# Optimization experiments

Hardware: AMD Instinct MI355X
Metric: run time of the kernel (lower is better)

Reference implementation:

```python
import jax, jax.numpy as jnp
import numpy as np

B, S, H, NH = 4, 2048, 256, 8
EPS = 1e-5


def setup_inputs() -> dict:
    key = jax.random.key(0)
    ks = jax.random.split(key, 12)
    p = lambda k, shape: (jax.random.normal(k, shape, jnp.float32) * 0.02)
    return {
        "x": jax.random.normal(ks[0], (B, S, H), jnp.float32),
        "lengths": jax.random.randint(ks[1], (B,), 0, S).astype(jnp.int32),
        "atten_in": jnp.zeros((1,), jnp.float32),
        "Wq": p(ks[2], (H, H)), "bq": jnp.zeros((H,), jnp.float32),
        "Wk": p(ks[3], (H, H)), "bk": jnp.zeros((H,), jnp.float32),
        "Wv": p(ks[4], (H, H)), "bv": jnp.zeros((H,), jnp.float32),
        "W1": p(ks[5], (H, H)), "b1": jnp.zeros((H,), jnp.float32),
        "W2": p(ks[6], (H, H)), "b2": jnp.zeros((H,), jnp.float32),
        "g1": jnp.ones((H,), jnp.float32), "beta1": jnp.zeros((H,), jnp.float32),
        "g2": jnp.ones((H,), jnp.float32), "beta2": jnp.zeros((H,), jnp.float32),
    }


def _layer_norm(x, g, b):
    mu = x.mean(-1, keepdims=True)
    var = ((x - mu) ** 2).mean(-1, keepdims=True)
    return (x - mu) / jnp.sqrt(var + EPS) * g + b


def reference(x, lengths, atten_in, Wq, bq, Wk, bk, Wv, bv, W1, b1, W2, b2, g1, beta1, g2, beta2):
    Bx, Sx, Hx = x.shape
    hd = Hx // NH
    # QKV projections, split heads -> [B, NH, S, hd]
    q = (x @ Wq + bq).reshape(Bx, Sx, NH, hd).transpose(0, 2, 1, 3)
    k = (x @ Wk + bk).reshape(Bx, Sx, NH, hd).transpose(0, 2, 1, 3)
    v = (x @ Wv + bv).reshape(Bx, Sx, NH, hd).transpose(0, 2, 1, 3)
    # NOTE: original scales by sqrt(hidden_size), not sqrt(head_dim)
    scores = jnp.einsum('bhqd,bhkd->bhqk', q, k) / np.sqrt(Hx).astype(np.float32)
    pos = jnp.arange(Sx)
    causal = pos[:, None] >= pos[None, :]                     # [S, S]
    row_ok = pos[None, :] < lengths[:, None]                  # [B, S]: mask query rows >= length
    head_ok = jnp.arange(NH)[None, :] < lengths[:, None]      # [B, NH]: original loop masks heads >= length
    mask = causal[None, None] & row_ok[:, None, :, None] & head_ok[:, :, None, None]
    neg = jnp.finfo(scores.dtype).min
    logits = jnp.where(mask, scores, neg)
    atten = jax.nn.softmax(logits, axis=-1)
    # original: masked_fill((atten > 0) == False, 0) -> fully masked rows (NaN in torch) become 0
    atten = jnp.where(mask, atten, 0.0)
    row_valid = mask.any(-1, keepdims=True)
    atten = jnp.where(row_valid, atten, 0.0)
    out = jnp.einsum('bhqk,bhkd->bhqd', atten, v).transpose(0, 2, 1, 3).reshape(Bx, Sx, Hx)
    atten_mean = atten.mean(axis=1)  # [B, S, S], detached in original
    out_1 = x + out  # dropout p=0 / eval mode -> identity
    out_1_norm = _layer_norm(out_1, g1, beta1)
    ff = jax.nn.gelu(out_1_norm @ W1 + b1, approximate=False) @ W2 + b2
    y_prim = _layer_norm(out_1_norm + ff, g2, beta2)
    return (y_prim, lengths, atten_mean)
```

## Files before the change

### kernel.cpp

```cpp
#include <hip/hip_runtime.h>
#include <math.h>

#define BB 4
#define SS 2048
#define HH 256
#define NHH 8
#define EPSV 1e-5f
#define NC 8
#define CHW (SS/NC)
#define NCO 4
#define QPRE 0.09016844005556021f

#if __has_builtin(__builtin_amdgcn_exp2f)
#define EXP2F(x) __builtin_amdgcn_exp2f(x)
#else
#define EXP2F(x) __expf((x) * 0.6931471805599453f)
#endif

typedef unsigned short ushortT;
typedef __attribute__((ext_vector_type(8))) short bf16x8;
typedef __attribute__((ext_vector_type(4))) float f32x4;

__device__ inline ushortT f2bf(float f) {
    union { float f; unsigned int u; } x; x.f = f;
    unsigned int r = x.u + 0x7FFFu + ((x.u >> 16) & 1u);
    return (ushortT)(r >> 16);
}
__device__ inline ushortT f2bf_rz(float f) {
    union { float f; unsigned int u; } x; x.f = f;
    return (ushortT)(x.u >> 16);
}
__device__ inline float bf2f(ushortT u) {
    union { unsigned int i; float f; } x; x.i = ((unsigned int)u) << 16;
    return x.f;
}

__global__ __launch_bounds__(256) void prep(const float* __restrict__ x,
        ushortT* __restrict__ xb, const int* __restrict__ L,
        float* __restrict__ out_len,
        const float* __restrict__ Wa, const float* __restrict__ Wb,
        const float* __restrict__ Wc, const float* __restrict__ Wd,
        const float* __restrict__ We, ushortT* __restrict__ Wtb) {
    const int bid = blockIdx.x;
    if (bid < 1024) {
        const int i = (bid * 256 + threadIdx.x) << 3;
        float4 v0 = *(const float4*)(x + i);
        float4 v1 = *(const float4*)(x + i + 4);
        bf16x8 o;
        o[0] = (short)f2bf(v0.x); o[1] = (short)f2bf(v0.y);
        o[2] = (short)f2bf(v0.z); o[3] = (short)f2bf(v0.w);
        o[4] = (short)f2bf(v1.x); o[5] = (short)f2bf(v1.y);
        o[6] = (short)f2bf(v1.z); o[7] = (short)f2bf(v1.w);
        *(bf16x8*)(xb + i) = o;
        if (bid == 0 && threadIdx.x < BB) out_len[threadIdx.x] = (float)L[threadIdx.x];
        return;
    }
    const int wb = bid - 1024;
    const int z = wb >> 6;
    const int rem = wb & 63;
    const int k0 = (rem >> 3) << 5, n0 = (rem & 7) << 5;
    const float* W = (z == 0) ? Wa : (z == 1) ? Wb : (z == 2) ? Wc : (z == 3) ? Wd : We;
    __shared__ float tile[32][33];
    const int t = threadIdx.x;
    const int r = t >> 3, c4 = (t & 7) << 2;
    float4 v = *(const float4*)(W + (size_t)(k0 + r) * HH + n0 + c4);
    tile[r][c4+0] = v.x; tile[r][c4+1] = v.y; tile[r][c4+2] = v.z; tile[r][c4+3] = v.w;
    __syncthreads();
    ushort4 o;
    o.x = f2bf(tile[c4+0][r]); o.y = f2bf(tile[c4+1][r]);
    o.z = f2bf(tile[c4+2][r]); o.w = f2bf(tile[c4+3][r]);
    *(ushort4*)(Wtb + (size_t)z * 65536 + (size_t)(n0 + r) * HH + k0 + c4) = o;
}

__global__ __launch_bounds__(256) void gemm_qkv(const ushortT* __restrict__ A,
        const ushortT* __restrict__ Wtb,
        const float* __restrict__ bq, const float* __restrict__ bk,
        const float* __restrict__ bv,
        ushortT* __restrict__ Qb, ushortT* __restrict__ Kb,
        ushortT* __restrict__ Vt) {
    __shared__ ushortT As[64][264];
    __shared__ ushortT Ws[64][264];
    const int wsel = blockIdx.y >> 2;
    const int n0 = (blockIdx.y & 3) << 6;
    const ushortT* Wt = Wtb + (size_t)wsel * 65536;
    const float* bias = (wsel == 0) ? bq : (wsel == 1) ? bk : bv;
    const int tid = threadIdx.x;
    const int m0 = blockIdx.x << 6;
    #pragma unroll
    for (int t = 0; t < 8; ++t) {
        const int f = t * 256 + tid;
        const int r = f >> 5;
        const int cc = (f & 31) << 3;
        *(bf16x8*)&As[r][cc] = *(const bf16x8*)(A + (size_t)(m0 + r) * HH + cc);
        *(bf16x8*)&Ws[r][cc] = *(const bf16x8*)(Wt + (size_t)(n0 + r) * HH + cc);
    }
    __syncthreads();
    const int w = tid >> 6, lane = tid & 63;
    const int lg = lane >> 4, lc = lane & 15;
    const int wr = (w & 1) << 5, wc = (w >> 1) << 5;
    f32x4 acc[2][2];
    const f32x4 z4 = {0.f, 0.f, 0.f, 0.f};
    acc[0][0] = z4; acc[0][1] = z4; acc[1][0] = z4; acc[1][1] = z4;
    #pragma unroll
    for (int k0 = 0; k0 < 256; k0 += 32) {
        bf16x8 a0 = *(const bf16x8*)&As[wr + lc][k0 + lg*8];
        bf16x8 a1 = *(const bf16x8*)&As[wr + 16 + lc][k0 + lg*8];
        bf16x8 b0 = *(const bf16x8*)&Ws[wc + lc][k0 + lg*8];
        bf16x8 b1 = *(const bf16x8*)&Ws[wc + 16 + lc][k0 + lg*8];
        acc[0][0] = __builtin_amdgcn_mfma_f32_16x16x32_bf16(a0, b0, acc[0][0], 0, 0, 0);
        acc[0][1] = __builtin_amdgcn_mfma_f32_16x16x32_bf16(a0, b1, acc[0][1], 0, 0, 0);
        acc[1][0] = __builtin_amdgcn_mfma_f32_16x16x32_bf16(a1, b0, acc[1][0], 0, 0, 0);
        acc[1][1] = __builtin_amdgcn_mfma_f32_16x16x32_bf16(a1, b1, acc[1][1], 0, 0, 0);
    }
    ushortT* Out = (wsel == 0) ? Qb : Kb;
    #pragma unroll
    for (int RH = 0; RH < 2; ++RH)
        #pragma unroll
        for (int CH = 0; CH < 2; ++CH) {
            const int col = n0 + wc + CH*16 + lc;
            const float bvv = bias[col];
            float v[4];
            #pragma unroll
            for (int r = 0; r < 4; ++r) {
                v[r] = acc[RH][CH][r] + bvv;
                if (wsel == 0) v[r] *= QPRE;
            }
            if (wsel < 2) {
                #pragma unroll
                for (int r = 0; r < 4; ++r) {
                    const int row = m0 + wr + RH*16 + lg*4 + r;
                    Out[(size_t)row * HH + col] = f2bf(v[r]);
                }
            } else {
                const int row0 = m0 + wr + RH*16 + lg*4;
                const int bidx = row0 >> 11, s0 = row0 & (SS - 1);
                ushort4 o;
                o.x = f2bf(v[0]); o.y = f2bf(v[1]); o.z = f2bf(v[2]); o.w = f2bf(v[3]);
                *(ushort4*)(Vt + ((size_t)(bidx * HH + col)) * SS + s0) = o;
            }
        }
}

template<int MODE>
__global__ __launch_bounds__(256) void gemm_mfma(const ushortT* __restrict__ A,
        const ushortT* __restrict__ Wt, const float* __restrict__ bias,
        void* __restrict__ Cv) {
    __shared__ ushortT As[64][264];
    __shared__ ushortT Ws[64][264];
    const int tid = threadIdx.x;
    const int m0 = blockIdx.x << 6;
    const int n0 = blockIdx.y << 6;
    #pragma unroll
    for (int t = 0; t < 8; ++t) {
        const int f = t * 256 + tid;
        const int r = f >> 5;
        const int cc = (f & 31) << 3;
        *(bf16x8*)&As[r][cc] = *(const bf16x8*)(A + (size_t)(m0 + r) * HH + cc);
        *(bf16x8*)&Ws[r][cc] = *(const bf16x8*)(Wt + (size_t)(n0 + r) * HH + cc);
    }
    __syncthreads();
    const int w = tid >> 6, lane = tid & 63;
    const int lg = lane >> 4, lc = lane & 15;
    const int wr = (w & 1) << 5, wc = (w >> 1) << 5;
    f32x4 acc[2][2];
    const f32x4 z4 = {0.f, 0.f, 0.f, 0.f};
    acc[0][0] = z4; acc[0][1] = z4; acc[1][0] = z4; acc[1][1] = z4;
    #pragma unroll
    for (int k0 = 0; k0 < 256; k0 += 32) {
        bf16x8 a0 = *(const bf16x8*)&As[wr + lc][k0 + lg*8];
        bf16x8 a1 = *(const bf16x8*)&As[wr + 16 + lc][k0 + lg*8];
        bf16x8 b0 = *(const bf16x8*)&Ws[wc + lc][k0 + lg*8];
        bf16x8 b1 = *(const bf16x8*)&Ws[wc + 16 + lc][k0 + lg*8];
        acc[0][0] = __builtin_amdgcn_mfma_f32_16x16x32_bf16(a0, b0, acc[0][0], 0, 0, 0);
        acc[0][1] = __builtin_amdgcn_mfma_f32_16x16x32_bf16(a0, b1, acc[0][1], 0, 0, 0);
        acc[1][0] = __builtin_amdgcn_mfma_f32_16x16x32_bf16(a1, b0, acc[1][0], 0, 0, 0);
        acc[1][1] = __builtin_amdgcn_mfma_f32_16x16x32_bf16(a1, b1, acc[1][1], 0, 0, 0);
    }
    #pragma unroll
    for (int RH = 0; RH < 2; ++RH)
        #pragma unroll
        for (int CH = 0; CH < 2; ++CH) {
            const int col = n0 + wc + CH*16 + lc;
            const float bv = bias[col];
            #pragma unroll
            for (int r = 0; r < 4; ++r) {
                const int row = m0 + wr + RH*16 + lg*4 + r;
                float v = acc[RH][CH][r] + bv;
                if (MODE == 2) v = 0.5f * v * (1.0f + erff(v * 0.70710678118f));
                if (MODE == 0) ((float*)Cv)[(size_t)row * HH + col] = v;
                else           ((ushortT*)Cv)[(size_t)row * HH + col] = f2bf(v);
            }
        }
}

__global__ __launch_bounds__(512) void attn_sums(const ushortT* __restrict__ Qb,
        const ushortT* __restrict__ Kb, const int* __restrict__ lengths,
        float* __restrict__ Psum) {
    const int b = blockIdx.z, c = blockIdx.y;
    const int i0 = (63 - blockIdx.x) << 5;
    const int len = lengths[b];
    const int jmax = min(i0 + 31, len - 1);
    const int jstart = c * CHW;
    if (i0 >= len || jstart > jmax) return;
    const int tid = threadIdx.x;
    const int w = tid >> 6, lane = tid & 63;
    const int lg = lane >> 4, lc = lane & 15;
    bf16x8 qf[2];
    #pragma unroll
    for (int RH = 0; RH < 2; ++RH)
        qf[RH] = *(const bf16x8*)(Qb + ((size_t)(b * SS + i0 + RH*16 + lc)) * HH + w*32 + lg*8);
    const f32x4 z4 = {0.f, 0.f, 0.f, 0.f};
    float lsum[2][4] = {};
    const int jend = min(jstart + CHW - 32, (jmax >> 5) << 5);
    bf16x8 kf0 = *(const bf16x8*)(Kb + ((size_t)(b * SS + jstart + lc)) * HH + w*32 + lg*8);
    bf16x8 kf1 = *(const bf16x8*)(Kb + ((size_t)(b * SS + jstart + 16 + lc)) * HH + w*32 + lg*8);
    for (int j0 = jstart; j0 <= jend; j0 += 32) {
        bf16x8 ck0 = kf0, ck1 = kf1;
        if (j0 + 32 <= jend) {
            kf0 = *(const bf16x8*)(Kb + ((size_t)(b * SS + j0 + 32 + lc)) * HH + w*32 + lg*8);
            kf1 = *(const bf16x8*)(Kb + ((size_t)(b * SS + j0 + 48 + lc)) * HH + w*32 + lg*8);
        }
        f32x4 s[2][2];
        #pragma unroll
        for (int RH = 0; RH < 2; ++RH) {
            s[RH][0] = __builtin_amdgcn_mfma_f32_16x16x32_bf16(qf[RH], ck0, z4, 0, 0, 0);
            s[RH][1] = __builtin_amdgcn_mfma_f32_16x16x32_bf16(qf[RH], ck1, z4, 0, 0, 0);
        }
        if (j0 < i0) {
            #pragma unroll
            for (int RH = 0; RH < 2; ++RH)
                #pragma unroll
                for (int r = 0; r < 4; ++r)
                    #pragma unroll
                    for (int CH = 0; CH < 2; ++CH)
                        lsum[RH][r] += EXP2F(s[RH][CH][r]);
        } else {
            #pragma unroll
            for (int RH = 0; RH < 2; ++RH)
                #pragma unroll
                for (int r = 0; r < 4; ++r) {
                    const int row = i0 + RH*16 + lg*4 + r;
                    #pragma unroll
                    for (int CH = 0; CH < 2; ++CH) {
                        const int j = j0 + CH*16 + lc;
                        lsum[RH][r] += (j <= row) ? EXP2F(s[RH][CH][r]) : 0.f;
                    }
                }
        }
    }
    #pragma unroll
    for (int RH = 0; RH < 2; ++RH)
        #pragma unroll
        for (int r = 0; r < 4; ++r) {
            float v = lsum[RH][r];
            v += __shfl_xor(v, 1); v += __shfl_xor(v, 2);
            v += __shfl_xor(v, 4); v += __shfl_xor(v, 8);
            if (lc == 0)
                Psum[((size_t)(c * BB + b) * NHH + w) * SS + i0 + RH*16 + lg*4 + r] = v;
        }
}

__global__ __launch_bounds__(512) void attn_pv(const ushortT* __restrict__ Qb,
        const ushortT* __restrict__ Kb, const ushortT* __restrict__ Vt,
        const int* __restrict__ lengths, const float* __restrict__ Psum,
        ushortT* __restrict__ OPart, float* __restrict__ out_mean) {
    __shared__ __align__(16) ushortT Pb[2][NHH][32][40];
    __shared__ float invS[NHH][32];
    const int b = blockIdx.z, cg = blockIdx.y;
    const int i0 = (63 - blockIdx.x) << 5;
    const int len = lengths[b];
    const int tid = threadIdx.x;
    const int mr = tid >> 4, mc = (tid & 15) << 1;
    float* meanrow = out_mean + ((size_t)(b * SS + i0 + mr)) * SS + mc;
    const int T = (i0 < len) ? ((min(i0 + 31, len - 1) >> 5) + 1) : 0;
    for (int t = T + ((cg - T) & (NCO - 1)); t < 64; t += NCO)
        *(float2*)(meanrow + (t << 5)) = make_float2(0.f, 0.f);
    const int q = T >> 2, r = T & (NCO - 1);
    const int t0 = cg * q + min(cg, r);
    const int t1 = t0 + q + (cg < r ? 1 : 0);
    if (t0 >= t1) return;
    if (tid < NHH * 32) {
        const int hh = tid >> 5, row = i0 + (tid & 31);
        float rv = 0.f;
        if (row < len && hh < len) {
            float s = 0.f;
            const int ncv = (row >> 8) + 1;
            for (int c2 = 0; c2 < ncv; ++c2)
                s += Psum[((size_t)(c2 * BB + b) * NHH + hh) * SS + row];
            rv = (s > 0.f) ? 1.0f / s : 0.f;
        }
        invS[hh][tid & 31] = rv;
    }
    __syncthreads();
    const int w = tid >> 6, lane = tid & 63;
    const int lg = lane >> 4, lc = lane & 15;
    bf16x8 qf[2];
    #pragma unroll
    for (int RH = 0; RH < 2; ++RH)
        qf[RH] = *(const bf16x8*)(Qb + ((size_t)(b * SS + i0 + RH*16 + lc)) * HH + w*32 + lg*8);
    float invv[2][4];
    #pragma unroll
    for (int RH = 0; RH < 2; ++RH)
        #pragma unroll
        for (int r2 = 0; r2 < 4; ++r2)
            invv[RH][r2] = invS[w][RH*16 + lg*4 + r2];
    float invh8[NHH];
    #pragma unroll
    for (int hh = 0; hh < NHH; ++hh)
        invh8[hh] = invS[hh][mr] * 0.125f;
    const f32x4 z4 = {0.f, 0.f, 0.f, 0.f};
    f32x4 O[2][2];
    O[0][0] = z4; O[0][1] = z4; O[1][0] = z4; O[1][1] = z4;
    const int jstart = t0 << 5;
    bf16x8 kf0 = *(const bf16x8*)(Kb + ((size_t)(b * SS + jstart + lc)) * HH + w*32 + lg*8);
    bf16x8 kf1 = *(const bf16x8*)(Kb + ((size_t)(b * SS + jstart + 16 + lc)) * HH + w*32 + lg*8);
    bf16x8 vf0 = *(const bf16x8*)(Vt + ((size_t)(b * HH + w*32 + lc)) * SS + jstart + lg*8);
    bf16x8 vf1 = *(const bf16x8*)(Vt + ((size_t)(b * HH + w*32 + 16 + lc)) * SS + jstart + lg*8);
    int par = 0;
    for (int t = t0; t < t1; ++t) {
        const int j0 = t << 5;
        bf16x8 ck0 = kf0, ck1 = kf1, cv0 = vf0, cv1 = vf1;
        if (t + 1 < t1) {
            kf0 = *(const bf16x8*)(Kb + ((size_t)(b * SS + j0 + 32 + lc)) * HH + w*32 + lg*8);
            kf1 = *(const bf16x8*)(Kb + ((size_t)(b * SS + j0 + 48 + lc)) * HH + w*32 + lg*8);
            vf0 = *(const bf16x8*)(Vt + ((size_t)(b * HH + w*32 + lc)) * SS + j0 + 32 + lg*8);
            vf1 = *(const bf16x8*)(Vt + ((size_t)(b * HH + w*32 + 16 + lc)) * SS + j0 + 32 + lg*8);
        }
        f32x4 s[2][2];
        #pragma unroll
        for (int RH = 0; RH < 2; ++RH) {
            s[RH][0] = __builtin_amdgcn_mfma_f32_16x16x32_bf16(qf[RH], ck0, z4, 0, 0, 0);
            s[RH][1] = __builtin_amdgcn_mfma_f32_16x16x32_bf16(qf[RH], ck1, z4, 0, 0, 0);
        }
        if (j0 < i0) {
            #pragma unroll
            for (int RH = 0; RH < 2; ++RH)
                #pragma unroll
                for (int CH = 0; CH < 2; ++CH)
                    #pragma unroll
                    for (int r2 = 0; r2 < 4; ++r2)
                        Pb[par][w][RH*16 + lg*4 + r2][CH*16 + lc] =
                            f2bf_rz(EXP2F(s[RH][CH][r2]));
        } else {
            #pragma unroll
            for (int RH = 0; RH < 2; ++RH)
                #pragma unroll
                for (int CH = 0; CH < 2; ++CH)
                    #pragma unroll
                    for (int r2 = 0; r2 < 4; ++r2) {
                        const int row = i0 + RH*16 + lg*4 + r2;
                        const int j = j0 + CH*16 + lc;
                        Pb[par][w][RH*16 + lg*4 + r2][CH*16 + lc] =
                            (j <= row) ? f2bf_rz(EXP2F(s[RH][CH][r2])) : (ushortT)0;
                    }
        }
        __syncthreads();
        #pragma unroll
        for (int RH = 0; RH < 2; ++RH) {
            bf16x8 pa = *(const bf16x8*)&Pb[par][w][RH*16 + lc][lg*8];
            O[RH][0] = __builtin_amdgcn_mfma_f32_16x16x32_bf16(pa, cv0, O[RH][0], 0, 0, 0);
            O[RH][1] = __builtin_amdgcn_mfma_f32_16x16x32_bf16(pa, cv1, O[RH][1], 0, 0, 0);
        }
        float m0 = 0.f, m1 = 0.f;
        #pragma unroll
        for (int ww = 0; ww < NHH; ++ww) {
            ushort2 t2 = *(const ushort2*)&Pb[par][ww][mr][mc];
            m0 += bf2f(t2.x) * invh8[ww]; m1 += bf2f(t2.y) * invh8[ww];
        }
        *(float2*)(meanrow + (j0)) = make_float2(m0, m1);
        par ^= 1;
    }
    ushortT* op = OPart + (size_t)cg * ((size_t)BB * SS * HH);
    #pragma unroll
    for (int RH = 0; RH < 2; ++RH)
        #pragma unroll
        for (int DH = 0; DH < 2; ++DH)
            #pragma unroll
            for (int r2 = 0; r2 < 4; ++r2)
                op[((size_t)(b * SS + i0 + RH*16 + lg*4 + r2)) * HH + w*32 + DH*16 + lc] =
                    f2bf(O[RH][DH][r2] * invv[RH][r2]);
}

__global__ __launch_bounds__(256) void add_ln_attn(const float* __restrict__ x,
        const ushortT* __restrict__ OPart, const int* __restrict__ lengths,
        const float* __restrict__ g, const float* __restrict__ beta,
        float* __restrict__ out, ushortT* __restrict__ outb) {
    const int row = blockIdx.x;
    const int c = threadIdx.x;
    const int i = row & (SS - 1);
    const int len = lengths[row >> 11];
    const size_t base = (size_t)row * 256;
    float v = x[base + c];
    if (i < len) {
        const int ncv = min(NCO, (i >> 5) + 1);
        for (int cc = 0; cc < ncv; ++cc)
            v += bf2f(OPart[(size_t)cc * ((size_t)BB * SS * HH) + base + c]);
    }
    __shared__ float red[8];
    float s = v;
    #pragma unroll
    for (int o = 32; o; o >>= 1) s += __shfl_down(s, o, 64);
    const int wid = c >> 6, lane = c & 63;
    if (lane == 0) red[wid] = s;
    __syncthreads();
    float mu = (red[0] + red[1] + red[2] + red[3]) * 0.00390625f;
    float d = v - mu;
    float q = d * d;
    #pragma unroll
    for (int o = 32; o; o >>= 1) q += __shfl_down(q, o, 64);
    if (lane == 0) red[4 + wid] = q;
    __syncthreads();
    float var = (red[4] + red[5] + red[6] + red[7]) * 0.00390625f;
    float res = d * rsqrtf(var + EPSV) * g[c] + beta[c];
    out[base + c] = res;
    outb[base + c] = f2bf(res);
}

__global__ __launch_bounds__(256) void add_ln(const float* __restrict__ A,
        const float* __restrict__ Bv, const float* __restrict__ g,
        const float* __restrict__ beta, float* __restrict__ out) {
    const int row = blockIdx.x;
    const int c = threadIdx.x;
    const size_t base = (size_t)row * 256;
    float v = A[base + c] + Bv[base + c];
    __shared__ float red[8];
    float s = v;
    #pragma unroll
    for (int o = 32; o; o >>= 1) s += __shfl_down(s, o, 64);
    const int wid = c >> 6, lane = c & 63;
    if (lane == 0) red[wid] = s;
    __syncthreads();
    float mu = (red[0] + red[1] + red[2] + red[3]) * 0.00390625f;
    float d = v - mu;
    float q = d * d;
    #pragma unroll
    for (int o = 32; o; o >>= 1) q += __shfl_down(q, o, 64);
    if (lane == 0) red[4 + wid] = q;
    __syncthreads();
    float var = (red[4] + red[5] + red[6] + red[7]) * 0.00390625f;
    out[base + c] = d * rsqrtf(var + EPSV) * g[c] + beta[c];
}

extern "C" void kernel_launch(void* const* d_in, const int* in_sizes, int n_in,
                              void* d_out, int out_size, void* d_ws, size_t ws_size,
                              hipStream_t stream) {
    const float* x   = (const float*)d_in[0];
    const int* lengths = (const int*)d_in[1];
    const float* Wq  = (const float*)d_in[3];
    const float* bq  = (const float*)d_in[4];
    const float* Wk  = (const float*)d_in[5];
    const float* bk  = (const float*)d_in[6];
    const float* Wv  = (const float*)d_in[7];
    const float* bv  = (const float*)d_in[8];
    const float* W1  = (const float*)d_in[9];
    const float* b1  = (const float*)d_in[10];
    const float* W2  = (const float*)d_in[11];
    const float* b2  = (const float*)d_in[12];
    const float* g1  = (const float*)d_in[13];
    const float* be1 = (const float*)d_in[14];
    const float* g2  = (const float*)d_in[15];
    const float* be2 = (const float*)d_in[16];
    float* out = (float*)d_out;
    float* ws  = (float*)d_ws;

    const size_t NELT = (size_t)BB * SS * HH;
    const size_t M1 = 1024 * 1024;

    ushortT* xb  = (ushortT*)ws;
    float*   Psum = ws;
    ushortT* Qbf = (ushortT*)(ws + M1);
    ushortT* Kbf = (ushortT*)(ws + 2 * M1);
    ushortT* Vtb = (ushortT*)(ws + 3 * M1);
    float*   X1N  = ws + 4 * M1;
    ushortT* Wtb = (ushortT*)(ws + 6 * M1);
    ushortT* OPart = (ushortT*)(ws + 7 * M1);
    ushortT* X1Nb = (ushortT*)ws;
    ushortT* F1b  = (ushortT*)(ws + M1);
    float*   F2   = ws + 2 * M1;

    float* out_y    = out;
    float* out_len  = out + NELT;
    float* out_mean = out + NELT + 4;

    prep<<<1344, 256, 0, stream>>>(x, xb, lengths, out_len, Wq, Wk, Wv, W1, W2, Wtb);
    gemm_qkv<<<dim3(128, 12), 256, 0, stream>>>(xb, Wtb, bq, bk, bv, Qbf, Kbf, Vtb);
    attn_sums<<<dim3(64, NC, 4), 512, 0, stream>>>(Qbf, Kbf, lengths, Psum);
    attn_pv<<<dim3(64, NCO, 4), 512, 0, stream>>>(Qbf, Kbf, Vtb, lengths, Psum, OPart, out_mean);
    add_ln_attn<<<8192, 256, 0, stream>>>(x, OPart, lengths, g1, be1, X1N, X1Nb);
    gemm_mfma<2><<<dim3(128, 4), 256, 0, stream>>>(X1Nb, Wtb + 3 * 65536, b1, (void*)F1b);
    gemm_mfma<0><<<dim3(128, 4), 256, 0, stream>>>(F1b,  Wtb + 4 * 65536, b2, (void*)F2);
    add_ln<<<8192, 256, 0, stream>>>(X1N, F2, g2, be2, out_y);
}
```

Measured before the change: 104.6 us.

## Fuse FFN GEMMs, GELU, residual and LayerNorm into one kernel

Replaces the two FFN GEMM launches and the final add+LayerNorm launch with a single kernel. Each 32-row block computes W1+GELU into shared memory, multiplies by W2, adds the residual and applies LayerNorm in registers, so the F1 and F2 intermediates never go through global memory. It also changes the zeroing of masked atten_mean columns to contiguous per-CTA ranges with float4 stores. The fused kernel launches only 256 blocks and reloads all weights per block, so it trades fewer launches and less intermediate traffic for lower parallelism and repeated weight loads.

```diff
diff --git a/kernel.cpp b/kernel.cpp
--- a/kernel.cpp
+++ b/kernel.cpp
@@ -141,58 +141,6 @@
         }
 }
 
-template<int MODE>
-__global__ __launch_bounds__(256) void gemm_mfma(const ushortT* __restrict__ A,
-        const ushortT* __restrict__ Wt, const float* __restrict__ bias,
-        void* __restrict__ Cv) {
-    __shared__ ushortT As[64][264];
-    __shared__ ushortT Ws[64][264];
-    const int tid = threadIdx.x;
-    const int m0 = blockIdx.x << 6;
-    const int n0 = blockIdx.y << 6;
-    #pragma unroll
-    for (int t = 0; t < 8; ++t) {
-        const int f = t * 256 + tid;
-        const int r = f >> 5;
-        const int cc = (f & 31) << 3;
-        *(bf16x8*)&As[r][cc] = *(const bf16x8*)(A + (size_t)(m0 + r) * HH + cc);
-        *(bf16x8*)&Ws[r][cc] = *(const bf16x8*)(Wt + (size_t)(n0 + r) * HH + cc);
-    }
-    __syncthreads();
-    const int w = tid >> 6, lane = tid & 63;
-    const int lg = lane >> 4, lc = lane & 15;
-    const int wr = (w & 1) << 5, wc = (w >> 1) << 5;
-    f32x4 acc[2][2];
-    const f32x4 z4 = {0.f, 0.f, 0.f, 0.f};
-    acc[0][0] = z4; acc[0][1] = z4; acc[1][0] = z4; acc[1][1] = z4;
-    #pragma unroll
-    for (int k0 = 0; k0 < 256; k0 += 32) {
-        bf16x8 a0 = *(const bf16x8*)&As[wr + lc][k0 + lg*8];
-        bf16x8 a1 = *(const bf16x8*)&As[wr + 16 + lc][k0 + lg*8];
-        bf16x8 b0 = *(const bf16x8*)&Ws[wc + lc][k0 + lg*8];
-        bf16x8 b1 = *(const bf16x8*)&Ws[wc + 16 + lc][k0 + lg*8];
-        acc[0][0] = __builtin_amdgcn_mfma_f32_16x16x32_bf16(a0, b0, acc[0][0], 0, 0, 0);
-        acc[0][1] = __builtin_amdgcn_mfma_f32_16x16x32_bf16(a0, b1, acc[0][1], 0, 0, 0);
-        acc[1][0] = __builtin_amdgcn_mfma_f32_16x16x32_bf16(a1, b0, acc[1][0], 0, 0, 0);
-        acc[1][1] = __builtin_amdgcn_mfma_f32_16x16x32_bf16(a1, b1, acc[1][1], 0, 0, 0);
-    }
-    #pragma unroll
-    for (int RH = 0; RH < 2; ++RH)
-        #pragma unroll
-        for (int CH = 0; CH < 2; ++CH) {
-            const int col = n0 + wc + CH*16 + lc;
-            const float bv = bias[col];
-            #pragma unroll
-            for (int r = 0; r < 4; ++r) {
-                const int row = m0 + wr + RH*16 + lg*4 + r;
-                float v = acc[RH][CH][r] + bv;
-                if (MODE == 2) v = 0.5f * v * (1.0f + erff(v * 0.70710678118f));
-                if (MODE == 0) ((float*)Cv)[(size_t)row * HH + col] = v;
-                else           ((ushortT*)Cv)[(size_t)row * HH + col] = f2bf(v);
-            }
-        }
-}
-
 __global__ __launch_bounds__(512) void attn_sums(const ushortT* __restrict__ Qb,
         const ushortT* __restrict__ Kb, const int* __restrict__ lengths,
         float* __restrict__ Psum) {
@@ -273,8 +221,15 @@
     const int mr = tid >> 4, mc = (tid & 15) << 1;
     float* meanrow = out_mean + ((size_t)(b * SS + i0 + mr)) * SS + mc;
     const int T = (i0 < len) ? ((min(i0 + 31, len - 1) >> 5) + 1) : 0;
-    for (int t = T + ((cg - T) & (NCO - 1)); t < 64; t += NCO)
-        *(float2*)(meanrow + (t << 5)) = make_float2(0.f, 0.f);
+    {
+        const int zc0 = T << 5;
+        const int zq = (SS - zc0) >> 2;
+        const int c0 = zc0 + cg * zq;
+        const int c1 = c0 + zq;
+        float* mrow0 = out_mean + ((size_t)(b * SS + i0 + mr)) * SS;
+        for (int cc2 = c0 + ((tid & 15) << 2); cc2 < c1; cc2 += 64)
+            *(float4*)(mrow0 + cc2) = make_float4(0.f, 0.f, 0.f, 0.f);
+    }
     const int q = T >> 2, r = T & (NCO - 1);
     const int t0 = cg * q + min(cg, r);
     const int t1 = t0 + q + (cg < r ? 1 : 0);
@@ -367,7 +322,7 @@
             ushort2 t2 = *(const ushort2*)&Pb[par][ww][mr][mc];
             m0 += bf2f(t2.x) * invh8[ww]; m1 += bf2f(t2.y) * invh8[ww];
         }
-        *(float2*)(meanrow + (j0)) = make_float2(m0, m1);
+        *(float2*)(meanrow + j0) = make_float2(m0, m1);
         par ^= 1;
     }
     ushortT* op = OPart + (size_t)cg * ((size_t)BB * SS * HH);
@@ -416,29 +371,146 @@
     outb[base + c] = f2bf(res);
 }
 
-__global__ __launch_bounds__(256) void add_ln(const float* __restrict__ A,
-        const float* __restrict__ Bv, const float* __restrict__ g,
-        const float* __restrict__ beta, float* __restrict__ out) {
-    const int row = blockIdx.x;
-    const int c = threadIdx.x;
-    const size_t base = (size_t)row * 256;
-    float v = A[base + c] + Bv[base + c];
-    __shared__ float red[8];
-    float s = v;
-    #pragma unroll
-    for (int o = 32; o; o >>= 1) s += __shfl_down(s, o, 64);
-    const int wid = c >> 6, lane = c & 63;
-    if (lane == 0) red[wid] = s;
-    __syncthreads();
-    float mu = (red[0] + red[1] + red[2] + red[3]) * 0.00390625f;
-    float d = v - mu;
-    float q = d * d;
-    #pragma unroll
-    for (int o = 32; o; o >>= 1) q += __shfl_down(q, o, 64);
-    if (lane == 0) red[4 + wid] = q;
-    __syncthreads();
-    float var = (red[4] + red[5] + red[6] + red[7]) * 0.00390625f;
-    out[base + c] = d * rsqrtf(var + EPSV) * g[c] + beta[c];
+__global__ __launch_bounds__(256) void ffn_fused(const ushortT* __restrict__ A,
+        const float* __restrict__ X1N,
+        const ushortT* __restrict__ W1t, const float* __restrict__ b1,
+        const ushortT* __restrict__ W2t, const float* __restrict__ b2,
+        const float* __restrict__ g2, const float* __restrict__ be2,
+        float* __restrict__ out) {
+    __shared__ ushortT Xs[32][264];
+    __shared__ ushortT Ws[64][264];
+    __shared__ ushortT F1s[32][264];
+    __shared__ float redA[4][16];
+    __shared__ float redB[4][16];
+    const int tid = threadIdx.x;
+    const int m0 = blockIdx.x << 5;
+    #pragma unroll
+    for (int t = 0; t < 4; ++t) {
+        const int f = t * 256 + tid;
+        const int rr = f >> 5, cc = (f & 31) << 3;
+        *(bf16x8*)&Xs[rr][cc] = *(const bf16x8*)(A + (size_t)(m0 + rr) * HH + cc);
+    }
+    const int w = tid >> 6, lane = tid & 63;
+    const int lg = lane >> 4, lc = lane & 15;
+    const int rw = (w & 1) << 4;
+    const int cw = (w >> 1) << 5;
+    const f32x4 z4 = {0.f, 0.f, 0.f, 0.f};
+    #pragma unroll
+    for (int nt = 0; nt < 4; ++nt) {
+        #pragma unroll
+        for (int t = 0; t < 8; ++t) {
+            const int f = t * 256 + tid;
+            const int rr = f >> 5, cc = (f & 31) << 3;
+            *(bf16x8*)&Ws[rr][cc] = *(const bf16x8*)(W1t + (size_t)(nt * 64 + rr) * HH + cc);
+        }
+        __syncthreads();
+        f32x4 acc[2]; acc[0] = z4; acc[1] = z4;
+        #pragma unroll
+        for (int k0 = 0; k0 < 256; k0 += 32) {
+            bf16x8 a  = *(const bf16x8*)&Xs[rw + lc][k0 + lg*8];
+            bf16x8 b0 = *(const bf16x8*)&Ws[cw + lc][k0 + lg*8];
+            bf16x8 b1v = *(const bf16x8*)&Ws[cw + 16 + lc][k0 + lg*8];
+            acc[0] = __builtin_amdgcn_mfma_f32_16x16x32_bf16(a, b0, acc[0], 0, 0, 0);
+            acc[1] = __builtin_amdgcn_mfma_f32_16x16x32_bf16(a, b1v, acc[1], 0, 0, 0);
+        }
+        #pragma unroll
+        for (int CH = 0; CH < 2; ++CH) {
+            const int col = nt * 64 + cw + CH * 16 + lc;
+            const float bv = b1[col];
+            #pragma unroll
+            for (int r = 0; r < 4; ++r) {
+                float v = acc[CH][r] + bv;
+                v = 0.5f * v * (1.0f + erff(v * 0.70710678118f));
+                F1s[rw + lg*4 + r][col] = f2bf(v);
+            }
+        }
+        __syncthreads();
+    }
+    f32x4 f2acc[4][2];
+    #pragma unroll
+    for (int nt = 0; nt < 4; ++nt) {
+        #pragma unroll
+        for (int t = 0; t < 8; ++t) {
+            const int f = t * 256 + tid;
+            const int rr = f >> 5, cc = (f & 31) << 3;
+            *(bf16x8*)&Ws[rr][cc] = *(const bf16x8*)(W2t + (size_t)(nt * 64 + rr) * HH + cc);
+        }
+        __syncthreads();
+        f2acc[nt][0] = z4; f2acc[nt][1] = z4;
+        #pragma unroll
+        for (int k0 = 0; k0 < 256; k0 += 32) {
+            bf16x8 a  = *(const bf16x8*)&F1s[rw + lc][k0 + lg*8];
+            bf16x8 b0 = *(const bf16x8*)&Ws[cw + lc][k0 + lg*8];
+            bf16x8 b1v = *(const bf16x8*)&Ws[cw + 16 + lc][k0 + lg*8];
+            f2acc[nt][0] = __builtin_amdgcn_mfma_f32_16x16x32_bf16(a, b0, f2acc[nt][0], 0, 0, 0);
+            f2acc[nt][1] = __builtin_amdgcn_mfma_f32_16x16x32_bf16(a, b1v, f2acc[nt][1], 0, 0, 0);
+        }
+        __syncthreads();
+    }
+    float v[4][2][4];
+    float s[4] = {0.f, 0.f, 0.f, 0.f};
+    #pragma unroll
+    for (int nt = 0; nt < 4; ++nt)
+        #pragma unroll
+        for (int CH = 0; CH < 2; ++CH) {
+            const int col = nt * 64 + cw + CH * 16 + lc;
+            const float bv = b2[col];
+            #pragma unroll
+            for (int r = 0; r < 4; ++r) {
+                const int row = m0 + rw + lg*4 + r;
+                float vv = f2acc[nt][CH][r] + bv + X1N[(size_t)row * HH + col];
+                v[nt][CH][r] = vv;
+                s[r] += vv;
+            }
+        }
+    #pragma unroll
+    for (int r = 0; r < 4; ++r) {
+        s[r] += __shfl_xor(s[r], 1); s[r] += __shfl_xor(s[r], 2);
+        s[r] += __shfl_xor(s[r], 4); s[r] += __shfl_xor(s[r], 8);
+    }
+    if (lc == 0) {
+        #pragma unroll
+        for (int r = 0; r < 4; ++r) redA[w][lg*4 + r] = s[r];
+    }
+    __syncthreads();
+    float mu[4];
+    #pragma unroll
+    for (int r = 0; r < 4; ++r)
+        mu[r] = (redA[w][lg*4 + r] + redA[w ^ 2][lg*4 + r]) * 0.00390625f;
+    float qs[4] = {0.f, 0.f, 0.f, 0.f};
+    #pragma unroll
+    for (int nt = 0; nt < 4; ++nt)
+        #pragma unroll
+        for (int CH = 0; CH < 2; ++CH)
+            #pragma unroll
+            for (int r = 0; r < 4; ++r) {
+                const float d = v[nt][CH][r] - mu[r];
+                qs[r] += d * d;
+            }
+    #pragma unroll
+    for (int r = 0; r < 4; ++r) {
+        qs[r] += __shfl_xor(qs[r], 1); qs[r] += __shfl_xor(qs[r], 2);
+        qs[r] += __shfl_xor(qs[r], 4); qs[r] += __shfl_xor(qs[r], 8);
+    }
+    if (lc == 0) {
+        #pragma unroll
+        for (int r = 0; r < 4; ++r) redB[w][lg*4 + r] = qs[r];
+    }
+    __syncthreads();
+    #pragma unroll
+    for (int r = 0; r < 4; ++r) {
+        const float var = (redB[w][lg*4 + r] + redB[w ^ 2][lg*4 + r]) * 0.00390625f;
+        const float rs = rsqrtf(var + EPSV);
+        const int row = m0 + rw + lg*4 + r;
+        #pragma unroll
+        for (int nt = 0; nt < 4; ++nt)
+            #pragma unroll
+            for (int CH = 0; CH < 2; ++CH) {
+                const int col = nt * 64 + cw + CH * 16 + lc;
+                out[(size_t)row * HH + col] =
+                    (v[nt][CH][r] - mu[r]) * rs * g2[col] + be2[col];
+            }
+    }
 }
 
 extern "C" void kernel_launch(void* const* d_in, const int* in_sizes, int n_in,
@@ -475,8 +547,6 @@
     ushortT* Wtb = (ushortT*)(ws + 6 * M1);
     ushortT* OPart = (ushortT*)(ws + 7 * M1);
     ushortT* X1Nb = (ushortT*)ws;
-    ushortT* F1b  = (ushortT*)(ws + M1);
-    float*   F2   = ws + 2 * M1;
 
     float* out_y    = out;
     float* out_len  = out + NELT;
@@ -487,7 +557,6 @@
     attn_sums<<<dim3(64, NC, 4), 512, 0, stream>>>(Qbf, Kbf, lengths, Psum);
     attn_pv<<<dim3(64, NCO, 4), 512, 0, stream>>>(Qbf, Kbf, Vtb, lengths, Psum, OPart, out_mean);
     add_ln_attn<<<8192, 256, 0, stream>>>(x, OPart, lengths, g1, be1, X1N, X1Nb);
-    gemm_mfma<2><<<dim3(128, 4), 256, 0, stream>>>(X1Nb, Wtb + 3 * 65536, b1, (void*)F1b);
-    gemm_mfma<0><<<dim3(128, 4), 256, 0, stream>>>(F1b,  Wtb + 4 * 65536, b2, (void*)F2);
-    add_ln<<<8192, 256, 0, stream>>>(X1N, F2, g2, be2, out_y);
-}
+    ffn_fused<<<256, 256, 0, stream>>>(X1Nb, X1N, Wtb + 3 * 65536, b1,
+                                       Wtb + 4 * 65536, b2, g2, be2, out_y);
+}
```

Measured after the change: 110.3 us. 1.05x slower.
